# Optimization experiments

Measured on AMD Instinct MI355X. Metric: run time of the kernel, lower is better.

Reference implementation:

```python
import jax, jax.numpy as jnp
import numpy as np

B, N, K = 4, 4096, 16      # batch, points, knn neighbors (knn_point(16, ...))
CIN, C = 9, 128            # in_channels = 3 + extra(6); block width
NCLS = 13


def setup_inputs():
    key = jax.random.key(0)
    ks = jax.random.split(key, 16)
    def w(i, shape):
        return jax.random.normal(ks[i], shape, jnp.float32) * 0.05
    return {
        "inputs": jax.random.normal(ks[0], (B, CIN, N), jnp.float32),
        "emb_w1": w(1, (C, CIN)),
        "emb_s1": jnp.ones((C,), jnp.float32),
        "emb_b1": jnp.zeros((C,), jnp.float32),
        "emb_w2": w(2, (C, C)),
        "emb_s2": jnp.ones((C,), jnp.float32),
        "emb_b2": jnp.zeros((C,), jnp.float32),
        "blk_wq": w(3, (3, C, C)),
        "blk_wk": w(4, (3, C, C)),
        "blk_wv": w(5, (3, C, C)),
        "blk_wpos": w(6, (3, C, 3)),
        "blk_wo": w(7, (3, C, C)),
        "blk_s": jnp.ones((3, C), jnp.float32),
        "blk_b": jnp.zeros((3, C), jnp.float32),
        "fuse_w": w(8, (1024, 3 * C)),
        "fuse_s": jnp.ones((1024,), jnp.float32),
        "fuse_b": jnp.zeros((1024,), jnp.float32),
        "cls_w1": w(9, (512, 3072)),
        "cls_bias1": jnp.zeros((512,), jnp.float32),
        "cls_s1": jnp.ones((512,), jnp.float32),
        "cls_sh1": jnp.zeros((512,), jnp.float32),
        "cls_w2": w(10, (256, 512)),
        "cls_bias2": jnp.zeros((256,), jnp.float32),
        "cls_s2": jnp.ones((256,), jnp.float32),
        "cls_sh2": jnp.zeros((256,), jnp.float32),
        "cls_w3": w(11, (NCLS, 256)),
        "cls_bias3": jnp.zeros((NCLS,), jnp.float32),
    }


def reference(inputs, emb_w1, emb_s1, emb_b1, emb_w2, emb_s2, emb_b2,
              blk_wq, blk_wk, blk_wv, blk_wpos, blk_wo, blk_s, blk_b,
              fuse_w, fuse_s, fuse_b,
              cls_w1, cls_bias1, cls_s1, cls_sh1,
              cls_w2, cls_bias2, cls_s2, cls_sh2,
              cls_w3, cls_bias3):
    xyz = inputs[:, :3, :]                                    # [B,3,N]
    # --- brute-force 16-NN (knn_point): pairwise sq. distances + top-k ---
    sq = jnp.sum(xyz * xyz, axis=1)                           # [B,N]
    d = sq[:, :, None] + sq[:, None, :] - 2.0 * jnp.einsum('bcn,bcm->bnm', xyz, xyz)
    _, idx = jax.lax.top_k(-d, K)                             # [B,N,K] nearest (self incl.)
    gather = jax.vmap(lambda t, i: t[i])                      # [N,c],[N,K] -> [N,K,c]

    def cbr(x, w, s, b):                                      # Conv1d(1x1,no bias)+BN(eval)+ReLU
        return jax.nn.relu(s[None, :, None] * jnp.einsum('oc,bcn->bon', w, x) + b[None, :, None])

    x = cbr(cbr(inputs, emb_w1, emb_s1, emb_b1), emb_w2, emb_s2, emb_b2)  # [B,C,N]

    xyz_t = jnp.transpose(xyz, (0, 2, 1))                     # [B,N,3]
    rel = xyz_t[:, :, None, :] - gather(xyz_t, idx)           # [B,N,K,3] relative coords
    scale = 1.0 / jnp.sqrt(jnp.asarray(C, jnp.float32))

    xs = []
    for i in range(3):                                        # PVDSA_Res blocks (point-branch local attention)
        q = jnp.einsum('oc,bcn->bno', blk_wq[i], x)           # [B,N,C]
        k = jnp.einsum('oc,bcn->bno', blk_wk[i], x)
        v = jnp.einsum('oc,bcn->bno', blk_wv[i], x)
        k_n = gather(k, idx)                                  # [B,N,K,C]
        v_n = gather(v, idx) + jnp.einsum('oc,bnkc->bnko', blk_wpos[i], rel)
        attn = jax.nn.softmax(jnp.einsum('bnc,bnkc->bnk', q, k_n) * scale, axis=-1)
        agg = jnp.einsum('bnk,bnkc->bnc', attn, v_n)
        y = jnp.einsum('oc,bnc->bon', blk_wo[i], agg)         # out projection -> [B,C,N]
        x = x + jax.nn.relu(blk_s[i][None, :, None] * y + blk_b[i][None, :, None])  # res=True
        xs.append(x)

    x = jnp.concatenate(xs, axis=1)                           # [B,3C,N]
    x = fuse_s[None, :, None] * jnp.einsum('oc,bcn->bon', fuse_w, x) + fuse_b[None, :, None]
    x = jnp.where(x > 0, x, 0.2 * x)                          # LeakyReLU(0.2) -> [B,1024,N]

    g = jnp.concatenate([jnp.max(x, axis=-1), jnp.mean(x, axis=-1)], axis=1)  # [B,2048]
    b_, _, n_ = x.shape
    x = jnp.concatenate([x, jnp.broadcast_to(g[:, :, None], (b_, g.shape[1], n_))], axis=1)  # [B,3072,N]

    def cbbr(x, w, bias, s, sh):                              # Conv1d(1x1,bias)+BN(eval)+ReLU
        return jax.nn.relu(s[None, :, None] * (jnp.einsum('oc,bcn->bon', w, x) + bias[None, :, None]) + sh[None, :, None])

    x = cbbr(x, cls_w1, cls_bias1, cls_s1, cls_sh1)           # Dropout = identity (eval)
    x = cbbr(x, cls_w2, cls_bias2, cls_s2, cls_sh2)
    return jnp.einsum('oc,bcn->bon', cls_w3, x) + cls_bias3[None, :, None]  # [B,NCLS,N]
```

## Files before the change

### kernel.cpp

```cpp
#include <hip/hip_runtime.h>


#define NB 4
#define NP 4096
#define NT 16384

#define SCRATCH_BYTES (132u*1024u*1024u)
__device__ __align__(256) unsigned char g_scratch[SCRATCH_BYTES];

typedef __attribute__((ext_vector_type(8))) short short8;
typedef __attribute__((ext_vector_type(4))) float f32x4;
typedef __attribute__((ext_vector_type(4))) unsigned short ushort4v;

__device__ __forceinline__ float bf2f(unsigned short u){
  unsigned int v = ((unsigned int)u) << 16;
  return __builtin_bit_cast(float, v);
}
__device__ __forceinline__ unsigned short f2bf(float f){
  unsigned int x = __builtin_bit_cast(unsigned int, f);
  x += 0x7fffu + ((x >> 16) & 1u);
  return (unsigned short)(x >> 16);
}
__device__ __forceinline__ float sq3(float x, float y, float z){
  return __fadd_rn(__fadd_rn(__fmul_rn(x,x), __fmul_rn(y,y)), __fmul_rn(z,z));
}

#define KINS4(a0,a1,a2,a3,dd) do{ float _d=(dd);\
  a3=fminf(fmaxf(a2,_d),a3); a2=fminf(fmaxf(a1,_d),a2);\
  a1=fminf(fmaxf(a0,_d),a1); a0=fminf(a0,_d);}while(0)

#define KDECLD float d0=3.0e38f,d1=3.0e38f,d2=3.0e38f,d3=3.0e38f,d4=3.0e38f,\
  d5=3.0e38f,d6=3.0e38f,d7=3.0e38f,d8=3.0e38f,d9=3.0e38f,d10=3.0e38f,\
  d11=3.0e38f,d12=3.0e38f,d13=3.0e38f,d14=3.0e38f,d15=3.0e38f
#define KINSD(dd) do{ float _d=(dd); \
  d15=fminf(fmaxf(d14,_d),d15); d14=fminf(fmaxf(d13,_d),d14); \
  d13=fminf(fmaxf(d12,_d),d13); d12=fminf(fmaxf(d11,_d),d12); \
  d11=fminf(fmaxf(d10,_d),d11); d10=fminf(fmaxf(d9 ,_d),d10); \
  d9 =fminf(fmaxf(d8 ,_d),d9 ); d8 =fminf(fmaxf(d7 ,_d),d8 ); \
  d7 =fminf(fmaxf(d6 ,_d),d7 ); d6 =fminf(fmaxf(d5 ,_d),d6 ); \
  d5 =fminf(fmaxf(d4 ,_d),d5 ); d4 =fminf(fmaxf(d3 ,_d),d4 ); \
  d3 =fminf(fmaxf(d2 ,_d),d3 ); d2 =fminf(fmaxf(d1 ,_d),d2 ); \
  d1 =fminf(fmaxf(d0 ,_d),d1 ); d0 =fminf(d0,_d); }while(0)

#define KDECL KDECLD; int i0=0,i1=0,i2=0,i3=0,i4=0,i5=0,i6=0,i7=0,i8=0,\
  i9=0,i10=0,i11=0,i12=0,i13=0,i14=0,i15=0
#define KINS(dd,mm) do{ float _d=(dd); int _m=(mm); \
  bool c15 = _d < d15; \
  bool c14 = _d < d14;  i15 = c14 ? i14 : (c15 ? _m : i15);  d15 = fminf(fmaxf(d14,_d), d15); \
  bool c13 = _d < d13;  i14 = c13 ? i13 : (c14 ? _m : i14);  d14 = fminf(fmaxf(d13,_d), d14); \
  bool c12 = _d < d12;  i13 = c12 ? i12 : (c13 ? _m : i13);  d13 = fminf(fmaxf(d12,_d), d13); \
  bool c11 = _d < d11;  i12 = c11 ? i11 : (c12 ? _m : i12);  d12 = fminf(fmaxf(d11,_d), d12); \
  bool c10 = _d < d10;  i11 = c10 ? i10 : (c11 ? _m : i11);  d11 = fminf(fmaxf(d10,_d), d11); \
  bool c9  = _d < d9;   i10 = c9  ? i9  : (c10 ? _m : i10);  d10 = fminf(fmaxf(d9 ,_d), d10); \
  bool c8  = _d < d8;   i9  = c8  ? i8  : (c9  ? _m : i9 );  d9  = fminf(fmaxf(d8 ,_d), d9 ); \
  bool c7  = _d < d7;   i8  = c7  ? i7  : (c8  ? _m : i8 );  d8  = fminf(fmaxf(d7 ,_d), d8 ); \
  bool c6  = _d < d6;   i7  = c6  ? i6  : (c7  ? _m : i7 );  d7  = fminf(fmaxf(d6 ,_d), d7 ); \
  bool c5  = _d < d5;   i6  = c5  ? i5  : (c6  ? _m : i6 );  d6  = fminf(fmaxf(d5 ,_d), d6 ); \
  bool c4  = _d < d4;   i5  = c4  ? i4  : (c5  ? _m : i5 );  d5  = fminf(fmaxf(d4 ,_d), d5 ); \
  bool c3  = _d < d3;   i4  = c3  ? i3  : (c4  ? _m : i4 );  d4  = fminf(fmaxf(d3 ,_d), d4 ); \
  bool c2  = _d < d2;   i3  = c2  ? i2  : (c3  ? _m : i3 );  d3  = fminf(fmaxf(d2 ,_d), d3 ); \
  bool c1  = _d < d1;   i2  = c1  ? i1  : (c2  ? _m : i2 );  d2  = fminf(fmaxf(d1 ,_d), d2 ); \
  bool c0  = _d < d0;   i1  = c0  ? i0  : (c1  ? _m : i1 );  d1  = fminf(fmaxf(d0 ,_d), d1 ); \
  i0 = c0 ? _m : i0;  d0 = fminf(d0,_d); }while(0)

struct CvtArgs {
  const float* src[8];
  unsigned dstOff[8];
  int n[8];
};
__global__ __launch_bounds__(256) void cvt_all(CvtArgs a)
{
  int y = blockIdx.y;
  const float* src = a.src[y];
  unsigned short* dst = (unsigned short*)(g_scratch + a.dstOff[y]);
  int n = a.n[y];
  if (y == 7){
    for (int i = blockIdx.x*256 + threadIdx.x; i < n; i += gridDim.x*256){
      int r = i >> 10, c = i & 1023;
      dst[i] = f2bf(src[(size_t)r*3072 + c]);
    }
  } else {
    for (int i = blockIdx.x*256 + threadIdx.x; i < n; i += gridDim.x*256)
      dst[i] = f2bf(src[i]);
  }
}

__global__ __launch_bounds__(256) void knn_p1(const float* __restrict__ in,
                                              unsigned pdOff)
{
  float* pdist = (float*)(g_scratch + pdOff);
  __shared__ float4 sp[256];
  int b = blockIdx.z, qc = blockIdx.x, cc = blockIdx.y;
  const float* xb = in + (size_t)b*9*NP;
  int base = cc*256;
  {
    int i = threadIdx.x;
    float x = xb[base+i], y = xb[NP+base+i], z = xb[2*NP+base+i];
    sp[i] = make_float4(x,y,z, x*x+y*y+z*z);
  }
  __syncthreads();
  int n = qc*256 + threadIdx.x;
  float xn=xb[n], yn=xb[NP+n], zn=xb[2*NP+n];
  float sqn = xn*xn + yn*yn + zn*zn;
  float A0=3e38f,A1=3e38f,A2=3e38f,A3=3e38f;
  float B0=3e38f,B1=3e38f,B2=3e38f,B3=3e38f;
  float C0=3e38f,C1=3e38f,C2=3e38f,C3=3e38f;
  float D0=3e38f,D1=3e38f,D2=3e38f,D3=3e38f;
  for (int mm=0; mm<256; mm+=4){
    float4 p0 = sp[mm], p1 = sp[mm+1], p2 = sp[mm+2], p3 = sp[mm+3];
    float e0 = sqn + p0.w - 2.f*(xn*p0.x + yn*p0.y + zn*p0.z);
    float e1 = sqn + p1.w - 2.f*(xn*p1.x + yn*p1.y + zn*p1.z);
    float e2 = sqn + p2.w - 2.f*(xn*p2.x + yn*p2.y + zn*p2.z);
    float e3 = sqn + p3.w - 2.f*(xn*p3.x + yn*p3.y + zn*p3.z);
    KINS4(A0,A1,A2,A3,e0);
    KINS4(B0,B1,B2,B3,e1);
    KINS4(C0,C1,C2,C3,e2);
    KINS4(D0,D1,D2,D3,e3);
  }
  size_t ob = ((size_t)(b*16+cc)*16)*NP + n;
  pdist[ob+ 0*(size_t)NP]=A0; pdist[ob+ 1*(size_t)NP]=A1; pdist[ob+ 2*(size_t)NP]=A2; pdist[ob+ 3*(size_t)NP]=A3;
  pdist[ob+ 4*(size_t)NP]=B0; pdist[ob+ 5*(size_t)NP]=B1; pdist[ob+ 6*(size_t)NP]=B2; pdist[ob+ 7*(size_t)NP]=B3;
  pdist[ob+ 8*(size_t)NP]=C0; pdist[ob+ 9*(size_t)NP]=C1; pdist[ob+10*(size_t)NP]=C2; pdist[ob+11*(size_t)NP]=C3;
  pdist[ob+12*(size_t)NP]=D0; pdist[ob+13*(size_t)NP]=D1; pdist[ob+14*(size_t)NP]=D2; pdist[ob+15*(size_t)NP]=D3;
}

__global__ __launch_bounds__(256) void knn_thr(unsigned pdOff, unsigned thrOff)
{
  const float* pdist = (const float*)(g_scratch + pdOff);
  float* thr = (float*)(g_scratch + thrOff);
  int t = blockIdx.x*256 + threadIdx.x;
  int b = t >> 12, n = t & 4095;
  KDECLD;
  for (int cc=0; cc<16; ++cc){
    size_t ob = ((size_t)(b*16+cc)*16)*NP + n;
    #pragma unroll
    for (int j=0;j<16;j++){ KINSD(pdist[ob + (size_t)j*NP]); }
  }
  thr[t] = d15*1.000002f + 2e-4f;
}

__global__ __launch_bounds__(256) void knn_p2(const float* __restrict__ in,
                                              unsigned thrOff, unsigned pdOff, unsigned piOff)
{
  const float* thr = (const float*)(g_scratch + thrOff);
  float* pdist = (float*)(g_scratch + pdOff);
  int*   pidx  = (int*)  (g_scratch + piOff);
  __shared__ float4 sp[256];
  int b = blockIdx.z, qc = blockIdx.x, cc = blockIdx.y;
  const float* xb = in + (size_t)b*9*NP;
  int base = cc*256;
  {
    int i = threadIdx.x;
    float x = xb[base+i], y = xb[NP+base+i], z = xb[2*NP+base+i];
    sp[i] = make_float4(x,y,z,sq3(x,y,z));
  }
  __syncthreads();
  int n = qc*256 + threadIdx.x;
  float xn=xb[n], yn=xb[NP+n], zn=xb[2*NP+n];
  float sqn = sq3(xn,yn,zn);
  float th = thr[(b<<12) + n];
  size_t o = ((size_t)((b*16 + cc)*NP + n))*16;
  int cnt = 0;
  for (int mm=0; mm<256; ++mm){
    float4 p = sp[mm];
    float dot = __fadd_rn(__fadd_rn(__fmul_rn(xn,p.x), __fmul_rn(yn,p.y)), __fmul_rn(zn,p.z));
    float d = __fsub_rn(__fadd_rn(sqn, p.w), __fmul_rn(2.0f, dot));
    if (d <= th && cnt < 16){
      pdist[o+cnt] = d;
      pidx[o+cnt] = base + mm;
      cnt++;
    }
  }
  if (cnt < 16) pdist[o+cnt] = 3.0e38f;
}

__global__ __launch_bounds__(64) void knn_mrg(unsigned pdOff, unsigned piOff, unsigned idxOff)
{
  const float* pdist = (const float*)(g_scratch + pdOff);
  const int*   pidx  = (const int*)  (g_scratch + piOff);
  int*         idxOut= (int*)(g_scratch + idxOff);
  int t = blockIdx.x*64 + threadIdx.x;
  int b = t >> 12, n = t & 4095;
  KDECL;
  for (int cc=0; cc<16; ++cc){
    size_t o = ((size_t)((b*16 + cc)*NP + n))*16;
    #pragma unroll 1
    for (int j=0;j<16;j++){
      float pd = pdist[o+j];
      if (pd >= 1.0e38f) break;
      KINS(pd, pidx[o+j]);
    }
  }
  idxOut[t*16+ 0]=i0;  idxOut[t*16+ 1]=i1;  idxOut[t*16+ 2]=i2;  idxOut[t*16+ 3]=i3;
  idxOut[t*16+ 4]=i4;  idxOut[t*16+ 5]=i5;  idxOut[t*16+ 6]=i6;  idxOut[t*16+ 7]=i7;
  idxOut[t*16+ 8]=i8;  idxOut[t*16+ 9]=i9;  idxOut[t*16+10]=i10; idxOut[t*16+11]=i11;
  idxOut[t*16+12]=i12; idxOut[t*16+13]=i13; idxOut[t*16+14]=i14; idxOut[t*16+15]=i15;
}

__global__ __launch_bounds__(256) void emb1_kernel(const float* __restrict__ in,
                                                   const float* __restrict__ w1,
                                                   const float* __restrict__ s1,
                                                   const float* __restrict__ b1,
                                                   unsigned x1Off)
{
  unsigned short* x1 = (unsigned short*)(g_scratch + x1Off);
  int og = blockIdx.y*32;
  __shared__ float wf[32*9], sf[32], bf_[32];
  for (int i = threadIdx.x; i < 32*9; i += 256) wf[i] = w1[og*9 + i];
  if (threadIdx.x < 32){ sf[threadIdx.x]=s1[og+threadIdx.x]; bf_[threadIdx.x]=b1[og+threadIdx.x]; }
  __syncthreads();
  int t = blockIdx.x*256 + threadIdx.x;
  int b = t >> 12, n = t & 4095;
  float v[9];
  #pragma unroll
  for (int c=0;c<9;c++) v[c] = in[((size_t)b*9 + c)*NP + n];
  for (int o=0;o<32;o+=2){
    float a0=0.f, a1=0.f;
    #pragma unroll
    for (int c=0;c<9;c++){ a0 += wf[o*9+c]*v[c]; a1 += wf[(o+1)*9+c]*v[c]; }
    a0 = fmaxf(sf[o]*a0 + bf_[o], 0.f);
    a1 = fmaxf(sf[o+1]*a1 + bf_[o+1], 0.f);
    unsigned pk = (unsigned)f2bf(a0) | ((unsigned)f2bf(a1) << 16);
    *(unsigned*)(x1 + (size_t)t*128 + og + o) = pk;
  }
}

enum { EPI_PLAIN=0, EPI_RELU_SB=1, EPI_RES=2, EPI_LEAKY=3, EPI_CLS=4 };

template<int EPI, bool EXB>
__device__ __forceinline__ void gemm_epi(
    f32x4 (&acc)[4][4], int M0, int T0, int r, int q,
    unsigned short* out, int outStride, int outOff,
    const float* sPtr, const float* bPtr,
    const float* extraIn, unsigned extraOffB, int extraStride,
    unsigned resOffB, int resStride, int resOff)
{
  #pragma unroll
  for (int i=0;i<4;i++){
    int m = M0 + i*16 + q*4;
    float sv[4], bv[4];
    if constexpr (EPI != EPI_PLAIN){
      #pragma unroll
      for (int u=0;u<4;u++){ sv[u]=sPtr[m+u]; bv[u]=bPtr[m+u]; }
    }
    #pragma unroll
    for (int j=0;j<4;j++){
      int token = T0 + j*16 + r;
      float ex[4];
      if constexpr (EPI == EPI_CLS){
        int bb = token >> 12;
        #pragma unroll
        for (int u=0;u<4;u++)
          ex[u] = EXB ? extraIn[bb*extraStride + m + u]
                      : ((const float*)(g_scratch + extraOffB))[bb*extraStride + m + u];
      }
      float resv[4];
      if constexpr (EPI == EPI_RES){
        const unsigned short* resPtr = (const unsigned short*)(g_scratch + resOffB);
        ushort4v rv = *(const ushort4v*)(resPtr + (size_t)token*resStride + resOff + m);
        #pragma unroll
        for (int u=0;u<4;u++) resv[u]=bf2f(rv[u]);
      }
      ushort4v ov;
      #pragma unroll
      for (int u=0;u<4;u++){
        float aa = acc[i][j][u];
        float vo;
        if constexpr (EPI == EPI_PLAIN)        vo = aa;
        else if constexpr (EPI == EPI_RELU_SB) vo = fmaxf(sv[u]*aa + bv[u], 0.f);
        else if constexpr (EPI == EPI_RES)     vo = resv[u] + fmaxf(sv[u]*aa + bv[u], 0.f);
        else if constexpr (EPI == EPI_LEAKY){  float tt = sv[u]*aa + bv[u]; vo = tt>0.f ? tt : 0.2f*tt; }
        else { vo = fmaxf(sv[u]*(aa + ex[u]) + bv[u], 0.f); }
        ov[u] = f2bf(vo);
      }
      *(ushort4v*)(out + (size_t)token*outStride + outOff + m) = ov;
    }
  }
}

template<int EPI, bool EXB>
__global__ __launch_bounds__(256) void gemm_lds(
    unsigned W0off, unsigned W1off, unsigned W2off,
    unsigned O0off, unsigned O1off, unsigned O2off,
    unsigned XoffB, int Xstride, int Xoff,
    int outStride, int outOff,
    const float* sPtr, const float* bPtr,
    const float* extraIn, unsigned extraOffB, int extraStride,
    unsigned resOffB, int resStride, int resOff,
    int K, int Astride)
{
  __shared__ unsigned short As[128*32];
  __shared__ unsigned short Bs[128*32];
  const unsigned short* X = (const unsigned short*)(g_scratch + XoffB);
  unsigned wOffB   = (blockIdx.z==0) ? W0off : ((blockIdx.z==1) ? W1off : W2off);
  unsigned outOffB = (blockIdx.z==0) ? O0off : ((blockIdx.z==1) ? O1off : O2off);
  const unsigned short* W = (const unsigned short*)(g_scratch + wOffB);
  unsigned short* out = (unsigned short*)(g_scratch + outOffB);
  int lin = blockIdx.x + gridDim.x*blockIdx.y;
  int bx = lin >> 7;
  int by = (lin & 7)*16 + ((lin >> 3) & 15);
  int M0 = bx*128, T0 = by*128;
  int t = threadIdx.x;
  int lane = t & 63, wave = t >> 6;
  int r = lane & 15, q = lane >> 4;
  int srow = t >> 2, schunk = t & 3;

  const unsigned short* Ag0 = W + (size_t)(M0 + srow)*Astride + schunk*8;
  const unsigned short* Ag1 = W + (size_t)(M0 + 64 + srow)*Astride + schunk*8;
  const unsigned short* Bg0 = X + (size_t)(T0 + srow)*Xstride + Xoff + schunk*8;
  const unsigned short* Bg1 = X + (size_t)(T0 + 64 + srow)*Xstride + Xoff + schunk*8;
  unsigned short* Aw0 = &As[srow*32 + schunk*8];
  unsigned short* Aw1 = &As[(64 + srow)*32 + schunk*8];
  unsigned short* Bw0 = &Bs[srow*32 + schunk*8];
  unsigned short* Bw1 = &Bs[(64 + srow)*32 + schunk*8];

  int Mw = (wave>>1)*64, Tw = (wave&1)*64;
  f32x4 acc[4][4];
  #pragma unroll
  for (int i=0;i<4;i++)
    #pragma unroll
    for (int j=0;j<4;j++)
      #pragma unroll
      for (int u=0;u<4;u++) acc[i][j][u] = 0.f;

  for (int k0=0; k0<K; k0+=32){
    short8 va0 = *(const short8*)(Ag0 + k0);
    short8 va1 = *(const short8*)(Ag1 + k0);
    short8 vb0 = *(const short8*)(Bg0 + k0);
    short8 vb1 = *(const short8*)(Bg1 + k0);
    if (k0) __syncthreads();
    *(short8*)Aw0 = va0; *(short8*)Aw1 = va1;
    *(short8*)Bw0 = vb0; *(short8*)Bw1 = vb1;
    __syncthreads();
    short8 a[4], bfr[4];
    #pragma unroll
    for (int i=0;i<4;i++) a[i]   = *(const short8*)(&As[(Mw + i*16 + r)*32 + q*8]);
    #pragma unroll
    for (int j=0;j<4;j++) bfr[j] = *(const short8*)(&Bs[(Tw + j*16 + r)*32 + q*8]);
    #pragma unroll
    for (int i=0;i<4;i++)
      #pragma unroll
      for (int j=0;j<4;j++)
        acc[i][j] = __builtin_amdgcn_mfma_f32_16x16x32_bf16(a[i], bfr[j], acc[i][j], 0, 0, 0);
  }
  gemm_epi<EPI,EXB>(acc, M0+Mw, T0+Tw, r, q, out, outStride, outOff,
                    sPtr, bPtr, extraIn, extraOffB, extraStride,
                    resOffB, resStride, resOff);
}

template<int EPI, bool EXB>
__global__ __launch_bounds__(128) void gemm_small(
    unsigned W0off, unsigned W1off, unsigned W2off,
    unsigned O0off, unsigned O1off, unsigned O2off,
    unsigned XoffB, int Xstride, int Xoff,
    int outStride, int outOff,
    const float* sPtr, const float* bPtr,
    const float* extraIn, unsigned extraOffB, int extraStride,
    unsigned resOffB, int resStride, int resOff,
    int K, int Astride)
{
  const unsigned short* X = (const unsigned short*)(g_scratch + XoffB);
  unsigned wOffB   = (blockIdx.z==0) ? W0off : ((blockIdx.z==1) ? W1off : W2off);
  unsigned outOffB = (blockIdx.z==0) ? O0off : ((blockIdx.z==1) ? O1off : O2off);
  const unsigned short* W = (const unsigned short*)(g_scratch + wOffB);
  unsigned short* out = (unsigned short*)(g_scratch + outOffB);
  int lane = threadIdx.x & 63, wave = threadIdx.x >> 6;
  int r = lane & 15, q = lane >> 4;
  int M0 = blockIdx.x*64;
  int T0 = blockIdx.y*128 + wave*64;

  f32x4 acc[4][4];
  #pragma unroll
  for (int i=0;i<4;i++)
    #pragma unroll
    for (int j=0;j<4;j++)
      #pragma unroll
      for (int u=0;u<4;u++) acc[i][j][u] = 0.f;

  const unsigned short* Arow[4]; const unsigned short* Brow[4];
  #pragma unroll
  for (int i=0;i<4;i++) Arow[i] = W + (size_t)(M0 + i*16 + r)*Astride + q*8;
  #pragma unroll
  for (int j=0;j<4;j++) Brow[j] = X + (size_t)(T0 + j*16 + r)*Xstride + Xoff + q*8;

  for (int k0=0; k0<K; k0+=32){
    short8 a[4], bfr[4];
    #pragma unroll
    for (int i=0;i<4;i++) a[i]   = *(const short8*)(Arow[i] + k0);
    #pragma unroll
    for (int j=0;j<4;j++) bfr[j] = *(const short8*)(Brow[j] + k0);
    #pragma unroll
    for (int i=0;i<4;i++)
      #pragma unroll
      for (int j=0;j<4;j++)
        acc[i][j] = __builtin_amdgcn_mfma_f32_16x16x32_bf16(a[i], bfr[j], acc[i][j], 0, 0, 0);
  }
  gemm_epi<EPI,EXB>(acc, M0, T0, r, q, out, outStride, outOff,
                    sPtr, bPtr, extraIn, extraOffB, extraStride,
                    resOffB, resStride, resOff);
}

__global__ __launch_bounds__(256) void attn_kernel(
  unsigned qOff, unsigned kOff, unsigned vOff, unsigned idxOff,
  const float* __restrict__ in, const float* __restrict__ wpos,
  unsigned aggOff)
{
  const unsigned short* Q  = (const unsigned short*)(g_scratch + qOff);
  const unsigned short* Kf = (const unsigned short*)(g_scratch + kOff);
  const unsigned short* V  = (const unsigned short*)(g_scratch + vOff);
  const int* idx           = (const int*)(g_scratch + idxOff);
  unsigned short* agg      = (unsigned short*)(g_scratch + aggOff);

  int lane = threadIdx.x & 63, wv = threadIdx.x >> 6;
  int t = blockIdx.x*4 + wv;
  int b = t >> 12, n = t & 4095;
  const float* xb = in + (size_t)b*9*NP;
  int c0 = lane*2;

  unsigned qv = *(const unsigned*)(Q + (size_t)t*128 + c0);
  float q0 = bf2f((unsigned short)(qv & 0xffff)), q1 = bf2f((unsigned short)(qv >> 16));
  float xn = xb[n], yn = xb[NP+n], zn = xb[2*NP+n];
  float wp00=wpos[c0*3+0],     wp01=wpos[c0*3+1],     wp02=wpos[c0*3+2];
  float wp10=wpos[(c0+1)*3+0], wp11=wpos[(c0+1)*3+1], wp12=wpos[(c0+1)*3+2];

  int mi[16]; float s[16];
  #pragma unroll
  for (int j=0;j<16;j++) mi[j] = idx[(size_t)t*16 + j] & 4095;
  #pragma unroll
  for (int j=0;j<16;j++){
    unsigned kv = *(const unsigned*)(Kf + ((size_t)(b<<12) + mi[j])*128 + c0);
    float p = q0*bf2f((unsigned short)(kv & 0xffff)) + q1*bf2f((unsigned short)(kv >> 16));
    #pragma unroll
    for (int o=32;o>=1;o>>=1) p += __shfl_xor(p, o, 64);
    s[j] = p;
  }
  const float scale = 0.08838834764831845f;
  float mx = s[0];
  #pragma unroll
  for (int j=1;j<16;j++) mx = fmaxf(mx, s[j]);
  float e[16], sum = 0.f;
  #pragma unroll
  for (int j=0;j<16;j++){ e[j] = __expf((s[j]-mx)*scale); sum += e[j]; }
  float inv = 1.f / sum;

  float a0=0.f, a1=0.f;
  #pragma unroll
  for (int j=0;j<16;j++){
    int m = mi[j];
    float w = e[j]*inv;
    unsigned vv = *(const unsigned*)(V + ((size_t)(b<<12) + m)*128 + c0);
    float rx = xn - xb[m];
    float ry = yn - xb[NP+m];
    float rz = zn - xb[2*NP+m];
    float p0 = wp00*rx + wp01*ry + wp02*rz;
    float p1 = wp10*rx + wp11*ry + wp12*rz;
    a0 += w*(bf2f((unsigned short)(vv & 0xffff)) + p0);
    a1 += w*(bf2f((unsigned short)(vv >> 16)) + p1);
  }
  unsigned pk = (unsigned)f2bf(a0) | ((unsigned)f2bf(a1) << 16);
  *(unsigned*)(agg + (size_t)t*128 + c0) = pk;
}

__global__ __launch_bounds__(256) void pool_part(unsigned xfOff, unsigned gpOff)
{
  const unsigned short* xf = (const unsigned short*)(g_scratch + xfOff);
  float* gp = (float*)(g_scratch + gpOff);
  int b = blockIdx.x >> 7, cblk = (blockIdx.x >> 3) & 15, seg = blockIdx.x & 7;
  int cl = threadIdx.x & 63, tg = threadIdx.x >> 6;
  int c = cblk*64 + cl;
  float mx = -3.0e38f, sm = 0.f;
  for (int n = seg*512 + tg; n < (seg+1)*512; n += 4){
    float v = bf2f(xf[((size_t)(b<<12) + n)*1024 + c]);
    mx = fmaxf(mx, v); sm += v;
  }
  __shared__ float smx[4][64], ssm[4][64];
  smx[tg][cl]=mx; ssm[tg][cl]=sm;
  __syncthreads();
  if (tg==0){
    #pragma unroll
    for (int k=1;k<4;k++){ mx = fmaxf(mx, smx[k][cl]); sm += ssm[k][cl]; }
    gp[((b*8 + seg)*2 + 0)*1024 + c] = mx;
    gp[((b*8 + seg)*2 + 1)*1024 + c] = sm;
  }
}
__global__ __launch_bounds__(256) void pool_final(unsigned gpOff, unsigned gOff)
{
  const float* gp = (const float*)(g_scratch + gpOff);
  float* g = (float*)(g_scratch + gOff);
  int b = blockIdx.x;
  for (int c = threadIdx.x; c < 1024; c += 256){
    float mx = -3.0e38f, sm = 0.f;
    #pragma unroll
    for (int seg=0; seg<8; ++seg){
      mx = fmaxf(mx, gp[((b*8 + seg)*2 + 0)*1024 + c]);
      sm += gp[((b*8 + seg)*2 + 1)*1024 + c];
    }
    g[b*2048 + c] = mx;
    g[b*2048 + 1024 + c] = sm * (1.f/4096.f);
  }
}

__global__ __launch_bounds__(256) void gterm_kernel(const float* __restrict__ w1,
                                                    const float* __restrict__ bias1,
                                                    unsigned gOff, unsigned gbOff)
{
  const float* g = (const float*)(g_scratch + gOff);
  float* gb = (float*)(g_scratch + gbOff);
  int b = blockIdx.x >> 3, og = (blockIdx.x & 7)*64;
  int ol = threadIdx.x & 63, cq = threadIdx.x >> 6;
  int o = og + ol;
  const float* wrow = w1 + (size_t)o*3072 + 1024 + cq*512;
  const float* gp = g + b*2048 + cq*512;
  float acc = 0.f;
  for (int c=0;c<512;c+=4){
    float4 wv4 = *(const float4*)(wrow + c);
    acc += wv4.x*gp[c] + wv4.y*gp[c+1] + wv4.z*gp[c+2] + wv4.w*gp[c+3];
  }
  __shared__ float sred[4][64];
  sred[cq][ol] = acc;
  __syncthreads();
  if (cq==0){
    acc += sred[1][ol] + sred[2][ol] + sred[3][ol];
    gb[b*512 + o] = acc + bias1[o];
  }
}

__global__ __launch_bounds__(256) void cls3_kernel(unsigned c2Off,
                                                   const float* __restrict__ w3,
                                                   const float* __restrict__ bias3,
                                                   float* __restrict__ outp)
{
  const unsigned short* c2 = (const unsigned short*)(g_scratch + c2Off);
  __shared__ float wf[13*256];
  __shared__ float bf3[13];
  for (int i=threadIdx.x;i<13*256;i+=256) wf[i]=w3[i];
  if (threadIdx.x < 13) bf3[threadIdx.x]=bias3[threadIdx.x];
  __syncthreads();
  int lane = threadIdx.x & 63, wv = threadIdx.x >> 6;
  int tl = lane >> 2, cq = lane & 3;
  int t = blockIdx.x*64 + wv*16 + tl;
  const unsigned short* xrow = c2 + (size_t)t*256 + cq*64;
  float acc[13];
  #pragma unroll
  for (int o=0;o<13;o++) acc[o]=0.f;
  for (int c=0;c<64;c+=8){
    short8 xv = *(const short8*)(xrow + c);
    float xs[8];
    #pragma unroll
    for (int u=0;u<8;u++) xs[u]=bf2f((unsigned short)xv[u]);
    #pragma unroll
    for (int o=0;o<13;o++){
      const float* wr = wf + o*256 + cq*64 + c;
      #pragma unroll
      for (int u=0;u<8;u++) acc[o] += wr[u]*xs[u];
    }
  }
  #pragma unroll
  for (int o=0;o<13;o++){
    acc[o] += __shfl_xor(acc[o], 1, 64);
    acc[o] += __shfl_xor(acc[o], 2, 64);
  }
  if (cq==0){
    int b = t >> 12, n = t & 4095;
    #pragma unroll
    for (int o=0;o<13;o++)
      outp[((size_t)b*13 + o)*NP + n] = acc[o] + bf3[o];
  }
}

extern "C" void kernel_launch(void* const* d_in, const int* in_sizes, int n_in,
                              void* d_out, int out_size, void* d_ws, size_t ws_size,
                              hipStream_t stream) {
  (void)in_sizes; (void)n_in; (void)out_size; (void)d_ws; (void)ws_size;
  const float* in      = (const float*)d_in[0];
  const float* emb_w1  = (const float*)d_in[1];
  const float* emb_s1  = (const float*)d_in[2];
  const float* emb_b1  = (const float*)d_in[3];
  const float* emb_w2  = (const float*)d_in[4];
  const float* emb_s2  = (const float*)d_in[5];
  const float* emb_b2  = (const float*)d_in[6];
  const float* blk_wq  = (const float*)d_in[7];
  const float* blk_wk  = (const float*)d_in[8];
  const float* blk_wv  = (const float*)d_in[9];
  const float* blk_wpos= (const float*)d_in[10];
  const float* blk_wo  = (const float*)d_in[11];
  const float* blk_s   = (const float*)d_in[12];
  const float* blk_b   = (const float*)d_in[13];
  const float* fuse_w  = (const float*)d_in[14];
  const float* fuse_s  = (const float*)d_in[15];
  const float* fuse_b  = (const float*)d_in[16];
  const float* cls_w1  = (const float*)d_in[17];
  const float* cls_b1  = (const float*)d_in[18];
  const float* cls_s1  = (const float*)d_in[19];
  const float* cls_sh1 = (const float*)d_in[20];
  const float* cls_w2  = (const float*)d_in[21];
  const float* cls_b2  = (const float*)d_in[22];
  const float* cls_s2  = (const float*)d_in[23];
  const float* cls_sh2 = (const float*)d_in[24];
  const float* cls_w3  = (const float*)d_in[25];
  const float* cls_b3  = (const float*)d_in[26];

  const unsigned MB = 1u<<20, KB = 1024u;
  const unsigned OFF_IDX   = 0;
  const unsigned OFF_WQ    = 1*MB;
  const unsigned OFF_WK    = 1*MB + 128*KB;
  const unsigned OFF_WV    = 1*MB + 256*KB;
  const unsigned OFF_WO    = 1*MB + 384*KB;
  const unsigned OFF_WEMB2 = 1*MB + 512*KB;
  const unsigned OFF_WFUSE = 1*MB + 576*KB;
  const unsigned OFF_WW1   = 3*MB;
  const unsigned OFF_WW2   = 4*MB;
  const unsigned OFF_X1    = 5*MB;
  const unsigned OFF_X0    = 9*MB;
  const unsigned OFF_XCAT  = 13*MB;
  const unsigned OFF_QB    = 25*MB;
  const unsigned OFF_KB    = 29*MB;
  const unsigned OFF_VB    = 33*MB;
  const unsigned OFF_AGG   = 37*MB;
  const unsigned OFF_XF    = 41*MB;
  const unsigned OFF_C1    = 73*MB;
  const unsigned OFF_C2    = 89*MB;
  const unsigned OFF_G     = 97*MB;
  const unsigned OFF_GB    = 97*MB + 64*KB;
  const unsigned OFF_GP    = 97*MB + 128*KB;
  const unsigned OFF_THR   = 97*MB + 512*KB;
  const unsigned OFF_PD    = 98*MB;
  const unsigned OFF_PI    = 114*MB;
  float* outp = (float*)d_out;

  CvtArgs ca;
  ca.src[0]=emb_w2;  ca.dstOff[0]=OFF_WEMB2; ca.n[0]=128*128;
  ca.src[1]=blk_wq;  ca.dstOff[1]=OFF_WQ;    ca.n[1]=3*128*128;
  ca.src[2]=blk_wk;  ca.dstOff[2]=OFF_WK;    ca.n[2]=3*128*128;
  ca.src[3]=blk_wv;  ca.dstOff[3]=OFF_WV;    ca.n[3]=3*128*128;
  ca.src[4]=blk_wo;  ca.dstOff[4]=OFF_WO;    ca.n[4]=3*128*128;
  ca.src[5]=fuse_w;  ca.dstOff[5]=OFF_WFUSE; ca.n[5]=1024*384;
  ca.src[6]=cls_w2;  ca.dstOff[6]=OFF_WW2;   ca.n[6]=256*512;
  ca.src[7]=cls_w1;  ca.dstOff[7]=OFF_WW1;   ca.n[7]=512*1024;
  cvt_all<<<dim3(64,8), 256, 0, stream>>>(ca);

  knn_p1<<<dim3(16,16,4), 256, 0, stream>>>(in, OFF_PD);
  knn_thr<<<dim3(64), 256, 0, stream>>>(OFF_PD, OFF_THR);
  knn_p2<<<dim3(16,16,4), 256, 0, stream>>>(in, OFF_THR, OFF_PD, OFF_PI);
  knn_mrg<<<dim3(256), 64, 0, stream>>>(OFF_PD, OFF_PI, OFF_IDX);
  emb1_kernel<<<dim3(64,4), 256, 0, stream>>>(in, emb_w1, emb_s1, emb_b1, OFF_X1);
  gemm_small<EPI_RELU_SB,false><<<dim3(2,128,1), 128, 0, stream>>>(
      OFF_WEMB2, OFF_WEMB2, OFF_WEMB2, OFF_X0, OFF_X0, OFF_X0,
      OFF_X1, 128, 0, 128, 0, emb_s2, emb_b2,
      nullptr, 0, 0, 0, 0, 0, 128, 128);
  for (int i=0;i<3;i++){
    unsigned wq = OFF_WQ + i*32768, wk = OFF_WK + i*32768;
    unsigned wv = OFF_WV + i*32768, wo = OFF_WO + i*32768;
    const float* wp = blk_wpos + i*128*3;
    const float* si = blk_s + i*128;
    const float* bi = blk_b + i*128;
    unsigned XiOff = (i==0) ? OFF_X0 : OFF_XCAT;
    int Xs = (i==0) ? 128 : 384;
    int Xo = (i==0) ? 0 : (i-1)*128;
    gemm_small<EPI_PLAIN,false><<<dim3(2,128,3), 128, 0, stream>>>(
        wq, wk, wv, OFF_QB, OFF_KB, OFF_VB,
        XiOff, Xs, Xo, 128, 0, nullptr, nullptr,
        nullptr, 0, 0, 0, 0, 0, 128, 128);
    attn_kernel<<<dim3(4096), 256, 0, stream>>>(OFF_QB, OFF_KB, OFF_VB, OFF_IDX, in, wp, OFF_AGG);
    gemm_small<EPI_RES,false><<<dim3(2,128,1), 128, 0, stream>>>(
        wo, wo, wo, OFF_XCAT, OFF_XCAT, OFF_XCAT,
        OFF_AGG, 128, 0, 384, i*128, si, bi,
        nullptr, 0, 0, XiOff, Xs, Xo, 128, 128);
  }
  gemm_lds<EPI_LEAKY,false><<<dim3(8,128,1), 256, 0, stream>>>(
      OFF_WFUSE, OFF_WFUSE, OFF_WFUSE, OFF_XF, OFF_XF, OFF_XF,
      OFF_XCAT, 384, 0, 1024, 0, fuse_s, fuse_b,
      nullptr, 0, 0, 0, 0, 0, 384, 384);
  pool_part<<<dim3(512), 256, 0, stream>>>(OFF_XF, OFF_GP);
  pool_final<<<dim3(4), 256, 0, stream>>>(OFF_GP, OFF_G);
  gterm_kernel<<<dim3(32), 256, 0, stream>>>(cls_w1, cls_b1, OFF_G, OFF_GB);
  gemm_lds<EPI_CLS,false><<<dim3(4,128,1), 256, 0, stream>>>(
      OFF_WW1, OFF_WW1, OFF_WW1, OFF_C1, OFF_C1, OFF_C1,
      OFF_XF, 1024, 0, 512, 0, cls_s1, cls_sh1,
      nullptr, OFF_GB, 512, 0, 0, 0, 1024, 1024);
  gemm_lds<EPI_CLS,true><<<dim3(2,128,1), 256, 0, stream>>>(
      OFF_WW2, OFF_WW2, OFF_WW2, OFF_C2, OFF_C2, OFF_C2,
      OFF_C1, 512, 0, 256, 0, cls_s2, cls_sh2,
      cls_b2, 0, 0, 0, 0, 0, 512, 512);
  cls3_kernel<<<dim3(256), 256, 0, stream>>>(OFF_C2, cls_w3, cls_b3, outp);
}
```

Baseline: 541.4 us.

## Stage small-GEMM tiles through LDS and widen attention to 16 lanes per point

The small 128-wide GEMMs now cooperatively load A and B tiles into shared memory with coalesced 16-byte loads, then feed MFMA from LDS. Previously each wave fetched its own strided rows straight from global memory. The attention kernel now gives each point 16 lanes with 8 channels each instead of a full 64-lane wave with 2 channels. This uses 16-byte gathers, cuts the shuffle reduction from 6 to 4 steps, and processes 4x more points per block. The GEMM change adds two barriers per K-step, and the attention change raises register use per lane.

```diff
diff --git a/kernel.cpp b/kernel.cpp
--- a/kernel.cpp
+++ b/kernel.cpp
@@ -349,7 +349,7 @@
 }
 
 template<int EPI, bool EXB>
-__global__ __launch_bounds__(128) void gemm_small(
+__global__ __launch_bounds__(128) void gemm_small_lds(
     unsigned W0off, unsigned W1off, unsigned W2off,
     unsigned O0off, unsigned O1off, unsigned O2off,
     unsigned XoffB, int Xstride, int Xoff,
@@ -359,16 +359,33 @@
     unsigned resOffB, int resStride, int resOff,
     int K, int Astride)
 {
+  __shared__ unsigned short As[64*32];
+  __shared__ unsigned short Bs[128*32];
   const unsigned short* X = (const unsigned short*)(g_scratch + XoffB);
   unsigned wOffB   = (blockIdx.z==0) ? W0off : ((blockIdx.z==1) ? W1off : W2off);
   unsigned outOffB = (blockIdx.z==0) ? O0off : ((blockIdx.z==1) ? O1off : O2off);
   const unsigned short* W = (const unsigned short*)(g_scratch + wOffB);
   unsigned short* out = (unsigned short*)(g_scratch + outOffB);
-  int lane = threadIdx.x & 63, wave = threadIdx.x >> 6;
+  int M0 = blockIdx.x*64, T0 = blockIdx.y*128;
+  int t = threadIdx.x;
+  int lane = t & 63, wave = t >> 6;
   int r = lane & 15, q = lane >> 4;
-  int M0 = blockIdx.x*64;
-  int T0 = blockIdx.y*128 + wave*64;
-
+  int srow = t >> 2, schunk = t & 3;
+
+  const unsigned short* Ag0 = W + (size_t)(M0 + srow)*Astride + schunk*8;
+  const unsigned short* Ag1 = W + (size_t)(M0 + 32 + srow)*Astride + schunk*8;
+  const unsigned short* Bg0 = X + (size_t)(T0 + srow)*Xstride + Xoff + schunk*8;
+  const unsigned short* Bg1 = X + (size_t)(T0 + 32 + srow)*Xstride + Xoff + schunk*8;
+  const unsigned short* Bg2 = X + (size_t)(T0 + 64 + srow)*Xstride + Xoff + schunk*8;
+  const unsigned short* Bg3 = X + (size_t)(T0 + 96 + srow)*Xstride + Xoff + schunk*8;
+  unsigned short* Aw0 = &As[srow*32 + schunk*8];
+  unsigned short* Aw1 = &As[(32 + srow)*32 + schunk*8];
+  unsigned short* Bw0 = &Bs[srow*32 + schunk*8];
+  unsigned short* Bw1 = &Bs[(32 + srow)*32 + schunk*8];
+  unsigned short* Bw2 = &Bs[(64 + srow)*32 + schunk*8];
+  unsigned short* Bw3 = &Bs[(96 + srow)*32 + schunk*8];
+
+  int Tw = wave*64;
   f32x4 acc[4][4];
   #pragma unroll
   for (int i=0;i<4;i++)
@@ -377,25 +394,30 @@
       #pragma unroll
       for (int u=0;u<4;u++) acc[i][j][u] = 0.f;
 
-  const unsigned short* Arow[4]; const unsigned short* Brow[4];
-  #pragma unroll
-  for (int i=0;i<4;i++) Arow[i] = W + (size_t)(M0 + i*16 + r)*Astride + q*8;
-  #pragma unroll
-  for (int j=0;j<4;j++) Brow[j] = X + (size_t)(T0 + j*16 + r)*Xstride + Xoff + q*8;
-
   for (int k0=0; k0<K; k0+=32){
+    short8 va0 = *(const short8*)(Ag0 + k0);
+    short8 va1 = *(const short8*)(Ag1 + k0);
+    short8 vb0 = *(const short8*)(Bg0 + k0);
+    short8 vb1 = *(const short8*)(Bg1 + k0);
+    short8 vb2 = *(const short8*)(Bg2 + k0);
+    short8 vb3 = *(const short8*)(Bg3 + k0);
+    if (k0) __syncthreads();
+    *(short8*)Aw0 = va0; *(short8*)Aw1 = va1;
+    *(short8*)Bw0 = vb0; *(short8*)Bw1 = vb1;
+    *(short8*)Bw2 = vb2; *(short8*)Bw3 = vb3;
+    __syncthreads();
     short8 a[4], bfr[4];
     #pragma unroll
-    for (int i=0;i<4;i++) a[i]   = *(const short8*)(Arow[i] + k0);
-    #pragma unroll
-    for (int j=0;j<4;j++) bfr[j] = *(const short8*)(Brow[j] + k0);
+    for (int i=0;i<4;i++) a[i]   = *(const short8*)(&As[(i*16 + r)*32 + q*8]);
+    #pragma unroll
+    for (int j=0;j<4;j++) bfr[j] = *(const short8*)(&Bs[(Tw + j*16 + r)*32 + q*8]);
     #pragma unroll
     for (int i=0;i<4;i++)
       #pragma unroll
       for (int j=0;j<4;j++)
         acc[i][j] = __builtin_amdgcn_mfma_f32_16x16x32_bf16(a[i], bfr[j], acc[i][j], 0, 0, 0);
   }
-  gemm_epi<EPI,EXB>(acc, M0, T0, r, q, out, outStride, outOff,
+  gemm_epi<EPI,EXB>(acc, M0, T0+Tw, r, q, out, outStride, outOff,
                     sPtr, bPtr, extraIn, extraOffB, extraStride,
                     resOffB, resStride, resOff);
 }
@@ -412,26 +434,35 @@
   unsigned short* agg      = (unsigned short*)(g_scratch + aggOff);
 
   int lane = threadIdx.x & 63, wv = threadIdx.x >> 6;
-  int t = blockIdx.x*4 + wv;
+  int lg = lane >> 4;
+  int cl = lane & 15;
+  int t = blockIdx.x*16 + wv*4 + lg;
   int b = t >> 12, n = t & 4095;
   const float* xb = in + (size_t)b*9*NP;
-  int c0 = lane*2;
-
-  unsigned qv = *(const unsigned*)(Q + (size_t)t*128 + c0);
-  float q0 = bf2f((unsigned short)(qv & 0xffff)), q1 = bf2f((unsigned short)(qv >> 16));
+  int c0 = cl*8;
+
+  short8 qv = *(const short8*)(Q + (size_t)t*128 + c0);
+  float qf[8];
+  #pragma unroll
+  for (int u=0;u<8;u++) qf[u] = bf2f((unsigned short)qv[u]);
   float xn = xb[n], yn = xb[NP+n], zn = xb[2*NP+n];
-  float wp00=wpos[c0*3+0],     wp01=wpos[c0*3+1],     wp02=wpos[c0*3+2];
-  float wp10=wpos[(c0+1)*3+0], wp11=wpos[(c0+1)*3+1], wp12=wpos[(c0+1)*3+2];
+  float wp[8][3];
+  #pragma unroll
+  for (int u=0;u<8;u++){
+    wp[u][0]=wpos[(c0+u)*3+0]; wp[u][1]=wpos[(c0+u)*3+1]; wp[u][2]=wpos[(c0+u)*3+2];
+  }
 
   int mi[16]; float s[16];
   #pragma unroll
   for (int j=0;j<16;j++) mi[j] = idx[(size_t)t*16 + j] & 4095;
   #pragma unroll
   for (int j=0;j<16;j++){
-    unsigned kv = *(const unsigned*)(Kf + ((size_t)(b<<12) + mi[j])*128 + c0);
-    float p = q0*bf2f((unsigned short)(kv & 0xffff)) + q1*bf2f((unsigned short)(kv >> 16));
-    #pragma unroll
-    for (int o=32;o>=1;o>>=1) p += __shfl_xor(p, o, 64);
+    short8 kv = *(const short8*)(Kf + ((size_t)(b<<12) + mi[j])*128 + c0);
+    float p = 0.f;
+    #pragma unroll
+    for (int u=0;u<8;u++) p += qf[u]*bf2f((unsigned short)kv[u]);
+    #pragma unroll
+    for (int o=8;o>=1;o>>=1) p += __shfl_xor(p, o, 64);
     s[j] = p;
   }
   const float scale = 0.08838834764831845f;
@@ -443,22 +474,27 @@
   for (int j=0;j<16;j++){ e[j] = __expf((s[j]-mx)*scale); sum += e[j]; }
   float inv = 1.f / sum;
 
-  float a0=0.f, a1=0.f;
+  float a[8];
+  #pragma unroll
+  for (int u=0;u<8;u++) a[u] = 0.f;
   #pragma unroll
   for (int j=0;j<16;j++){
     int m = mi[j];
     float w = e[j]*inv;
-    unsigned vv = *(const unsigned*)(V + ((size_t)(b<<12) + m)*128 + c0);
+    short8 vvv = *(const short8*)(V + ((size_t)(b<<12) + m)*128 + c0);
     float rx = xn - xb[m];
     float ry = yn - xb[NP+m];
     float rz = zn - xb[2*NP+m];
-    float p0 = wp00*rx + wp01*ry + wp02*rz;
-    float p1 = wp10*rx + wp11*ry + wp12*rz;
-    a0 += w*(bf2f((unsigned short)(vv & 0xffff)) + p0);
-    a1 += w*(bf2f((unsigned short)(vv >> 16)) + p1);
-  }
-  unsigned pk = (unsigned)f2bf(a0) | ((unsigned)f2bf(a1) << 16);
-  *(unsigned*)(agg + (size_t)t*128 + c0) = pk;
+    #pragma unroll
+    for (int u=0;u<8;u++){
+      float pos = wp[u][0]*rx + wp[u][1]*ry + wp[u][2]*rz;
+      a[u] += w*(bf2f((unsigned short)vvv[u]) + pos);
+    }
+  }
+  short8 st;
+  #pragma unroll
+  for (int u=0;u<8;u++) st[u] = (short)f2bf(a[u]);
+  *(short8*)(agg + (size_t)t*128 + c0) = st;
 }
 
 __global__ __launch_bounds__(256) void pool_part(unsigned xfOff, unsigned gpOff)
@@ -644,7 +680,7 @@
   knn_p2<<<dim3(16,16,4), 256, 0, stream>>>(in, OFF_THR, OFF_PD, OFF_PI);
   knn_mrg<<<dim3(256), 64, 0, stream>>>(OFF_PD, OFF_PI, OFF_IDX);
   emb1_kernel<<<dim3(64,4), 256, 0, stream>>>(in, emb_w1, emb_s1, emb_b1, OFF_X1);
-  gemm_small<EPI_RELU_SB,false><<<dim3(2,128,1), 128, 0, stream>>>(
+  gemm_small_lds<EPI_RELU_SB,false><<<dim3(2,128,1), 128, 0, stream>>>(
       OFF_WEMB2, OFF_WEMB2, OFF_WEMB2, OFF_X0, OFF_X0, OFF_X0,
       OFF_X1, 128, 0, 128, 0, emb_s2, emb_b2,
       nullptr, 0, 0, 0, 0, 0, 128, 128);
@@ -657,12 +693,12 @@
     unsigned XiOff = (i==0) ? OFF_X0 : OFF_XCAT;
     int Xs = (i==0) ? 128 : 384;
     int Xo = (i==0) ? 0 : (i-1)*128;
-    gemm_small<EPI_PLAIN,false><<<dim3(2,128,3), 128, 0, stream>>>(
+    gemm_small_lds<EPI_PLAIN,false><<<dim3(2,128,3), 128, 0, stream>>>(
         wq, wk, wv, OFF_QB, OFF_KB, OFF_VB,
         XiOff, Xs, Xo, 128, 0, nullptr, nullptr,
         nullptr, 0, 0, 0, 0, 0, 128, 128);
-    attn_kernel<<<dim3(4096), 256, 0, stream>>>(OFF_QB, OFF_KB, OFF_VB, OFF_IDX, in, wp, OFF_AGG);
-    gemm_small<EPI_RES,false><<<dim3(2,128,1), 128, 0, stream>>>(
+    attn_kernel<<<dim3(1024), 256, 0, stream>>>(OFF_QB, OFF_KB, OFF_VB, OFF_IDX, in, wp, OFF_AGG);
+    gemm_small_lds<EPI_RES,false><<<dim3(2,128,1), 128, 0, stream>>>(
         wo, wo, wo, OFF_XCAT, OFF_XCAT, OFF_XCAT,
         OFF_AGG, 128, 0, 384, i*128, si, bi,
         nullptr, 0, 0, XiOff, Xs, Xo, 128, 128);
```

After: 513.7 us. -5.1%, faster.
